# Optimization experiments

Measured on AMD Instinct MI355X. Metric: run time of the kernel, lower is better.

The kernel has to match this reference:

```python
import jax, jax.numpy as jnp
import numpy as np

N = 98304        # total nodes (= 16384 graphs * act_dim 6)
E = 1572864      # edges (avg degree 16)
C = 64           # in_channels
H = 32           # hidden_size
ACT = 6          # act_dim


def setup_inputs() -> dict:
    key = jax.random.key(0)
    ks = jax.random.split(key, 11)
    s = lambda fan: 1.0 / np.sqrt(fan)
    return {
        "state": jax.random.normal(ks[0], (N, C), jnp.float32),
        "edge_index": jax.random.randint(ks[1], (2, E), 0, N, dtype=jnp.int64),
        "conv_W": jax.random.normal(ks[2], (C, C), jnp.float32) * s(C),
        "conv_b": jax.random.normal(ks[3], (C,), jnp.float32) * 0.01,
        "W1": jax.random.normal(ks[4], (C, H), jnp.float32) * s(C),
        "b1": jax.random.normal(ks[5], (H,), jnp.float32) * 0.01,
        "W2": jax.random.normal(ks[6], (H, H), jnp.float32) * s(H),
        "b2": jax.random.normal(ks[7], (H,), jnp.float32) * 0.01,
        "W3": jax.random.normal(ks[8], (H, 1), jnp.float32) * s(H),
        "b3": jax.random.normal(ks[9], (1,), jnp.float32) * 0.01,
    }


def gcn_conv(x, edge_index, W, b):
    # PyG GCNConv: add self-loops, symmetric normalization D^-1/2 (A+I) D^-1/2 (X W) + b
    loops = jnp.arange(N, dtype=edge_index.dtype)
    src = jnp.concatenate([edge_index[0], loops])  # [E+N]
    dst = jnp.concatenate([edge_index[1], loops])  # [E+N]
    deg = jax.ops.segment_sum(jnp.ones(E + N, x.dtype), dst, num_segments=N)
    dinv = jax.lax.rsqrt(deg)                      # deg >= 1 due to self-loops
    norm = dinv[src] * dinv[dst]                   # [E+N]
    h = x @ W                                      # [N, C]
    msg = h[src] * norm[:, None]                   # gather + scale
    return jax.ops.segment_sum(msg, dst, num_segments=N) + b


def reference(state, edge_index, conv_W, conv_b, W1, b1, W2, b2, W3, b3):
    out = jax.nn.relu(gcn_conv(state, edge_index, conv_W, conv_b))
    x = out + state                                # residual
    x = x.reshape(-1, ACT, C)                      # [num_graphs, act_dim, C]
    x = jax.nn.relu(x @ W1 + b1)
    x = jax.nn.relu(x @ W2 + b2)
    x = jax.nn.softplus(x @ W3 + b3)
    concentration = x.squeeze(-1) + 1e-20          # [num_graphs, act_dim]
    return concentration
```

## Files before the change

### kernel.cpp

```cpp
#include <hip/hip_runtime.h>
#include <math.h>

#define Nn 98304
#define Ee 1572864
#define Cc 64
#define Hh 32
#define HB 256
#define EPB (Ee / HB)
#define NST 384
#define SN 256
#define CAP_ST 4800
#define GN 64


__device__ __forceinline__ int detect64(const void* ei) {
    const unsigned int* u = (const unsigned int*)ei;
    int is64 = 1;
    #pragma unroll
    for (int i = 0; i < 16; ++i) is64 &= (u[2 * i + 1] == 0u);
    return is64;
}

__device__ __forceinline__ int load_idx(const void* ei, long e, int is64) {
    if (is64) return (int)((const long long*)ei)[e];
    return ((const int*)ei)[e];
}

__device__ __forceinline__ unsigned short f2bf(float x) {
    union { float f; unsigned int u; } v; v.f = x;
    unsigned int r = v.u + 0x7FFFu + ((v.u >> 16) & 1u);
    return (unsigned short)(r >> 16);
}

__device__ __forceinline__ void acc_u4(float a[8], uint4 u) {
    union { unsigned int i; float f; } w;
    w.i = u.x << 16;         a[0] += w.f;
    w.i = u.x & 0xFFFF0000u; a[1] += w.f;
    w.i = u.y << 16;         a[2] += w.f;
    w.i = u.y & 0xFFFF0000u; a[3] += w.f;
    w.i = u.z << 16;         a[4] += w.f;
    w.i = u.z & 0xFFFF0000u; a[5] += w.f;
    w.i = u.w << 16;         a[6] += w.f;
    w.i = u.w & 0xFFFF0000u; a[7] += w.f;
}
__device__ __forceinline__ void set_u4(float a[8], uint4 u) {
    union { unsigned int i; float f; } w;
    w.i = u.x << 16;         a[0] = w.f;
    w.i = u.x & 0xFFFF0000u; a[1] = w.f;
    w.i = u.y << 16;         a[2] = w.f;
    w.i = u.y & 0xFFFF0000u; a[3] = w.f;
    w.i = u.z << 16;         a[4] = w.f;
    w.i = u.z & 0xFFFF0000u; a[5] = w.f;
    w.i = u.w << 16;         a[6] = w.f;
    w.i = u.w & 0xFFFF0000u; a[7] = w.f;
}

__global__ __launch_bounds__(1024) void k_p1(const void* __restrict__ ei,
                                             unsigned int* __restrict__ aux,
                                             unsigned int* __restrict__ ebuf) {
    __shared__ unsigned int hl[NST];
    __shared__ unsigned int cur[NST];
    int t = threadIdx.x, b = blockIdx.x;
    if (t < NST) hl[t] = 0;
    __syncthreads();
    int is64 = detect64(ei);
    long e0 = (long)b * EPB;
    #pragma unroll
    for (int i = 0; i < EPB / 1024; ++i) {
        int d = load_idx(ei, (long)Ee + e0 + i * 1024 + t, is64);
        atomicAdd(&hl[d >> 8], 1u);
    }
    __syncthreads();
    if (t < NST) cur[t] = hl[t];
    __syncthreads();
    for (int s = 1; s < NST; s <<= 1) {
        unsigned int v = (t < NST && t >= s) ? cur[t - s] : 0u;
        __syncthreads();
        if (t < NST) cur[t] += v;
        __syncthreads();
    }
    if (t < NST) {
        unsigned int ex = cur[t] - hl[t];
        aux[(long)b * NST + t] = ex | (hl[t] << 16);
        cur[t] = ex;
    }
    __syncthreads();
    #pragma unroll
    for (int i = 0; i < EPB / 1024; ++i) {
        long e = e0 + i * 1024 + t;
        int s = load_idx(ei, e, is64);
        int d = load_idx(ei, (long)Ee + e, is64);
        unsigned int pos = atomicAdd(&cur[d >> 8], 1u);
        ebuf[(long)b * EPB + pos] = (unsigned int)s | ((unsigned int)(d & (SN - 1)) << 17);
    }
}

__global__ __launch_bounds__(512) void k_p2(const unsigned int* __restrict__ aux,
                                            const unsigned int* __restrict__ ebuf,
                                            unsigned int* __restrict__ rowOff,
                                            unsigned int* __restrict__ rowEnd,
                                            float* __restrict__ dinv,
                                            unsigned int* __restrict__ srcs) {
    __shared__ unsigned int stage[CAP_ST];
    __shared__ unsigned int rbI[HB];
    __shared__ unsigned int rof[HB];
    __shared__ unsigned int cnt[SN];
    __shared__ unsigned int sc[SN];
    __shared__ unsigned int cur[SN];
    int t = threadIdx.x, st = blockIdx.x;
    if (t < HB) {
        unsigned int av = aux[(long)t * NST + st];
        rof[t] = av & 0xFFFFu;
        rbI[t] = av >> 16;
    }
    if (t < SN) cnt[t] = 0;
    __syncthreads();
    for (int s = 1; s < HB; s <<= 1) {
        unsigned int v = (t < HB && t >= s) ? rbI[t - s] : 0u;
        __syncthreads();
        if (t < HB) rbI[t] += v;
        __syncthreads();
    }
    int total = (int)rbI[HB - 1];
    for (int i = t; i < total; i += 512) {
        int lo = 0, hi = HB - 1;
        while (lo < hi) {
            int mid = (lo + hi) >> 1;
            if (rbI[mid] > (unsigned int)i) hi = mid; else lo = mid + 1;
        }
        unsigned int ex = lo ? rbI[lo - 1] : 0u;
        stage[i] = ebuf[(long)lo * EPB + rof[lo] + ((unsigned int)i - ex)];
    }
    __syncthreads();
    for (int i = t; i < total; i += 512)
        atomicAdd(&cnt[stage[i] >> 17], 1u);
    __syncthreads();
    if (t < SN) sc[t] = cnt[t];
    __syncthreads();
    #pragma unroll
    for (int off = 1; off < SN; off <<= 1) {
        unsigned int v = (t < SN && t >= off) ? sc[t - off] : 0u;
        __syncthreads();
        if (t < SN) sc[t] += v;
        __syncthreads();
    }
    if (t < SN) {
        unsigned int start = (unsigned int)(st * CAP_ST) + sc[t] - cnt[t];
        rowOff[(long)st * SN + t] = start;
        rowEnd[(long)st * SN + t] = start + cnt[t];
        cur[t] = start;
        dinv[(long)st * SN + t] = rsqrtf((float)(cnt[t] + 1));
    }
    __syncthreads();
    for (int i = t; i < total; i += 512) {
        unsigned int u = stage[i];
        unsigned int pos = atomicAdd(&cur[u >> 17], 1u);
        srcs[pos] = u & 0x1FFFFu;
    }
}

__global__ __launch_bounds__(256) void k_gemm(const float* __restrict__ state,
                                              const float* __restrict__ W,
                                              const float* __restrict__ dinv,
                                              unsigned short* __restrict__ gb) {
    __shared__ float Wl[64 * 64];
    __shared__ float Al[64 * 68];
    int t = threadIdx.x;
    long n0 = (long)blockIdx.x * 64;

    const float4* W4 = (const float4*)W;
    float4* Wl4 = (float4*)Wl;
    #pragma unroll
    for (int i = 0; i < 4; ++i) Wl4[i * 256 + t] = W4[i * 256 + t];

    const float4* S4 = (const float4*)(state) + n0 * 16;
    #pragma unroll
    for (int i = 0; i < 4; ++i) {
        int f4 = t + i * 256;
        int r = f4 >> 4, k0 = (f4 & 15) * 4;
        *(float4*)(Al + r * 68 + k0) = S4[f4];
    }
    __syncthreads();

    int r0 = (t >> 4) * 4;
    int c0 = (t & 15) * 4;
    float acc[4][4] = {{0.f}};
    #pragma unroll
    for (int kk = 0; kk < 64; kk += 4) {
        float4 a4[4], w4[4];
        #pragma unroll
        for (int i = 0; i < 4; ++i) a4[i] = *(const float4*)(Al + (r0 + i) * 68 + kk);
        #pragma unroll
        for (int j = 0; j < 4; ++j) w4[j] = *(const float4*)(Wl + (kk + j) * 64 + c0);
        const float* aa = (const float*)a4;
        const float* ww = (const float*)w4;
        #pragma unroll
        for (int i = 0; i < 4; ++i)
            #pragma unroll
            for (int j = 0; j < 4; ++j) {
                float av = aa[i * 4 + j];
                #pragma unroll
                for (int c = 0; c < 4; ++c)
                    acc[i][c] = fmaf(av, ww[j * 4 + c], acc[i][c]);
            }
    }
    #pragma unroll
    for (int i = 0; i < 4; ++i) {
        long n = n0 + r0 + i;
        float dv = dinv[n];
        ushort4 o;
        o.x = f2bf(acc[i][0] * dv); o.y = f2bf(acc[i][1] * dv);
        o.z = f2bf(acc[i][2] * dv); o.w = f2bf(acc[i][3] * dv);
        *(ushort4*)(gb + n * 64 + c0) = o;
    }
}

__global__ __launch_bounds__(512) void k_gf(const unsigned int* __restrict__ rowOff,
                                            const unsigned int* __restrict__ rowEnd,
                                            const unsigned int* __restrict__ srcs,
                                            const unsigned short* __restrict__ gb,
                                            const float* __restrict__ dinv,
                                            const float* __restrict__ state,
                                            const float* __restrict__ conv_b,
                                            const float* __restrict__ W1,
                                            const float* __restrict__ b1,
                                            const float* __restrict__ W2,
                                            const float* __restrict__ b2,
                                            const float* __restrict__ W3,
                                            const float* __restrict__ b3,
                                            float* __restrict__ out) {
    __shared__ float sa[GN * 68];
    __shared__ float hs[GN * 34];
    __shared__ float sW1[Cc * Hh];
    __shared__ float sW2[Hh * Hh];
    __shared__ float sW3[Hh], sb1[Hh], sb2[Hh], scb[Cc];
    __shared__ float sb3;
    int t = threadIdx.x;
    int wave = t >> 6, lane = t & 63;
    long n0 = (long)blockIdx.x * GN;

    for (int i = t; i < Cc * Hh; i += 512) sW1[i] = W1[i];
    for (int i = t; i < Hh * Hh; i += 512) sW2[i] = W2[i];
    if (t < Hh) { sW3[t] = W3[t]; sb1[t] = b1[t]; sb2[t] = b2[t]; }
    if (t >= 64 && t < 128) scb[t - 64] = conv_b[t - 64];
    if (t == 511) sb3 = b3[0];
    __syncthreads();

    {
        int g = lane >> 3;
        int cs = lane & 7;
        int j = wave * 8 + g;
        long n = n0 + j;
        int ptr = (int)rowOff[n];
        int end = (int)rowEnd[n];
        float dv = dinv[n];
        const uint4* gb4 = (const uint4*)gb;

        float a[8];
        set_u4(a, gb4[n * 8 + cs]);

        int cnt = end - ptr;
        uint4 r0, r1, r2, r3;
        if (cnt >= 4) {
            int s0 = (int)srcs[ptr];
            int s1 = (int)srcs[ptr + 1];
            int s2 = (int)srcs[ptr + 2];
            int s3 = (int)srcs[ptr + 3];
            r0 = gb4[(long)s0 * 8 + cs];
            r1 = gb4[(long)s1 * 8 + cs];
            r2 = gb4[(long)s2 * 8 + cs];
            r3 = gb4[(long)s3 * 8 + cs];
        }
        while (cnt >= 8) {
            int t0 = (int)srcs[ptr + 4];
            int t1 = (int)srcs[ptr + 5];
            int t2 = (int)srcs[ptr + 6];
            int t3 = (int)srcs[ptr + 7];
            acc_u4(a, r0); acc_u4(a, r1);
            acc_u4(a, r2); acc_u4(a, r3);
            r0 = gb4[(long)t0 * 8 + cs];
            r1 = gb4[(long)t1 * 8 + cs];
            r2 = gb4[(long)t2 * 8 + cs];
            r3 = gb4[(long)t3 * 8 + cs];
            ptr += 4; cnt -= 4;
        }
        if (cnt >= 4) {
            acc_u4(a, r0); acc_u4(a, r1);
            acc_u4(a, r2); acc_u4(a, r3);
            ptr += 4; cnt -= 4;
        }
        while (cnt > 0) {
            int s0 = (int)srcs[ptr];
            uint4 u0 = gb4[(long)s0 * 8 + cs];
            acc_u4(a, u0);
            ++ptr; --cnt;
        }

        float* r = sa + j * 68 + cs * 8;
        float4 lo, hi;
        lo.x = a[0] * dv; lo.y = a[1] * dv; lo.z = a[2] * dv; lo.w = a[3] * dv;
        hi.x = a[4] * dv; hi.y = a[5] * dv; hi.z = a[6] * dv; hi.w = a[7] * dv;
        *(float4*)r = lo;
        *(float4*)(r + 4) = hi;
    }
    __builtin_amdgcn_wave_barrier();

    {
        int j = t >> 3, o = t & 7;
        long n = n0 + j;
        int k0 = o * 8;
        const float4* sp4 = (const float4*)(state + n * 64 + k0);
        float4 s0 = sp4[0], s1 = sp4[1];
        float* r = sa + j * 68 + k0;
        r[0] = fmaxf(r[0] + scb[k0 + 0], 0.f) + s0.x;
        r[1] = fmaxf(r[1] + scb[k0 + 1], 0.f) + s0.y;
        r[2] = fmaxf(r[2] + scb[k0 + 2], 0.f) + s0.z;
        r[3] = fmaxf(r[3] + scb[k0 + 3], 0.f) + s0.w;
        r[4] = fmaxf(r[4] + scb[k0 + 4], 0.f) + s1.x;
        r[5] = fmaxf(r[5] + scb[k0 + 5], 0.f) + s1.y;
        r[6] = fmaxf(r[6] + scb[k0 + 6], 0.f) + s1.z;
        r[7] = fmaxf(r[7] + scb[k0 + 7], 0.f) + s1.w;
    }
    __builtin_amdgcn_wave_barrier();

    {
        int j = t >> 3, o = t & 7;
        int c0 = o * 4;
        float a0 = sb1[c0], a1 = sb1[c0 + 1], a2 = sb1[c0 + 2], a3 = sb1[c0 + 3];
        #pragma unroll
        for (int k = 0; k < Cc; ++k) {
            float xv = sa[j * 68 + k];
            float4 w = *(const float4*)(sW1 + k * Hh + c0);
            a0 = fmaf(xv, w.x, a0); a1 = fmaf(xv, w.y, a1);
            a2 = fmaf(xv, w.z, a2); a3 = fmaf(xv, w.w, a3);
        }
        float* r = hs + j * 34 + c0;
        r[0] = fmaxf(a0, 0.f); r[1] = fmaxf(a1, 0.f);
        r[2] = fmaxf(a2, 0.f); r[3] = fmaxf(a3, 0.f);
    }
    __builtin_amdgcn_wave_barrier();

    {
        int j = t >> 3, o = t & 7;
        int c0 = o * 4;
        float a0 = sb2[c0], a1 = sb2[c0 + 1], a2 = sb2[c0 + 2], a3 = sb2[c0 + 3];
        #pragma unroll
        for (int k = 0; k < Hh; ++k) {
            float xv = hs[j * 34 + k];
            float4 w = *(const float4*)(sW2 + k * Hh + c0);
            a0 = fmaf(xv, w.x, a0); a1 = fmaf(xv, w.y, a1);
            a2 = fmaf(xv, w.z, a2); a3 = fmaf(xv, w.w, a3);
        }
        float* r = sa + j * 68 + c0;
        r[0] = fmaxf(a0, 0.f); r[1] = fmaxf(a1, 0.f);
        r[2] = fmaxf(a2, 0.f); r[3] = fmaxf(a3, 0.f);
    }
    __builtin_amdgcn_wave_barrier();

    {
        int g = lane >> 3, o = lane & 7;
        int j = wave * 8 + g;
        int k0 = o * 4;
        float y = 0.f;
        #pragma unroll
        for (int k = 0; k < 4; ++k) y = fmaf(sa[j * 68 + k0 + k], sW3[k0 + k], y);
        y += __shfl_xor(y, 1, 64);
        y += __shfl_xor(y, 2, 64);
        y += __shfl_xor(y, 4, 64);
        if (o == 0) {
            y += sb3;
            float sp = fmaxf(y, 0.f) + log1pf(expf(-fabsf(y)));
            out[n0 + j] = sp + 1e-20f;
        }
    }
}

extern "C" void kernel_launch(void* const* d_in, const int* in_sizes, int n_in,
                              void* d_out, int out_size, void* d_ws, size_t ws_size,
                              hipStream_t stream) {
    const float* state  = (const float*)d_in[0];
    const void*  ei     = d_in[1];
    const float* conv_W = (const float*)d_in[2];
    const float* conv_b = (const float*)d_in[3];
    const float* W1 = (const float*)d_in[4];
    const float* b1 = (const float*)d_in[5];
    const float* W2 = (const float*)d_in[6];
    const float* b2 = (const float*)d_in[7];
    const float* W3 = (const float*)d_in[8];
    const float* b3 = (const float*)d_in[9];
    float* out = (float*)d_out;

    float*          dinv   = (float*)d_ws;
    unsigned short* gb     = (unsigned short*)(dinv + Nn);
    unsigned int*   rowOff = (unsigned int*)(gb + (size_t)Nn * 64);
    unsigned int*   rowEnd = rowOff + Nn;
    unsigned int*   aux    = rowEnd + Nn;
    unsigned int*   ebuf   = aux + (size_t)HB * NST;
    unsigned int*   srcs   = ebuf + Ee;

    k_p1<<<HB, 1024, 0, stream>>>(ei, aux, ebuf);
    k_p2<<<NST, 512, 0, stream>>>(aux, ebuf, rowOff, rowEnd, dinv, srcs);
    k_gemm<<<Nn / 64, 256, 0, stream>>>(state, conv_W, dinv, gb);
    k_gf<<<Nn / GN, 512, 0, stream>>>(rowOff, rowEnd, srcs, gb, dinv, state, conv_b,
                                      W1, b1, W2, b2, W3, b3, out);
}
```

Baseline: 172.1 us.

## Sort nodes by degree within block, deepen gather prefetch, use packed float2 accumulation

Each block now ranks its 64 nodes by in-degree and assigns them to wave lanes in sorted order, so the eight nodes sharing a wave have similar edge counts and less divergence. The gather loop now keeps two groups of four row loads in flight (eight outstanding) instead of one, to hide more memory latency. Accumulation uses 2-wide float vectors, which may let the compiler emit packed adds. The cost is an extra rank-sort phase, a block-wide barrier in place of the wave barrier, and higher register pressure.

```diff
diff --git a/kernel.cpp b/kernel.cpp
--- a/kernel.cpp
+++ b/kernel.cpp
@@ -12,6 +12,8 @@
 #define CAP_ST 4800
 #define GN 64
 
+typedef float v2f __attribute__((ext_vector_type(2)));
+
 
 __device__ __forceinline__ int detect64(const void* ei) {
     const unsigned int* u = (const unsigned int*)ei;
@@ -32,27 +34,17 @@
     return (unsigned short)(r >> 16);
 }
 
-__device__ __forceinline__ void acc_u4(float a[8], uint4 u) {
-    union { unsigned int i; float f; } w;
-    w.i = u.x << 16;         a[0] += w.f;
-    w.i = u.x & 0xFFFF0000u; a[1] += w.f;
-    w.i = u.y << 16;         a[2] += w.f;
-    w.i = u.y & 0xFFFF0000u; a[3] += w.f;
-    w.i = u.z << 16;         a[4] += w.f;
-    w.i = u.z & 0xFFFF0000u; a[5] += w.f;
-    w.i = u.w << 16;         a[6] += w.f;
-    w.i = u.w & 0xFFFF0000u; a[7] += w.f;
-}
-__device__ __forceinline__ void set_u4(float a[8], uint4 u) {
-    union { unsigned int i; float f; } w;
-    w.i = u.x << 16;         a[0] = w.f;
-    w.i = u.x & 0xFFFF0000u; a[1] = w.f;
-    w.i = u.y << 16;         a[2] = w.f;
-    w.i = u.y & 0xFFFF0000u; a[3] = w.f;
-    w.i = u.z << 16;         a[4] = w.f;
-    w.i = u.z & 0xFFFF0000u; a[5] = w.f;
-    w.i = u.w << 16;         a[6] = w.f;
-    w.i = u.w & 0xFFFF0000u; a[7] = w.f;
+__device__ __forceinline__ v2f up2(unsigned int u) {
+    union { unsigned int i; float f; } lo, hi;
+    lo.i = u << 16; hi.i = u & 0xFFFF0000u;
+    v2f r; r.x = lo.f; r.y = hi.f;
+    return r;
+}
+__device__ __forceinline__ void accv(v2f A[4], uint4 u) {
+    A[0] += up2(u.x); A[1] += up2(u.y); A[2] += up2(u.z); A[3] += up2(u.w);
+}
+__device__ __forceinline__ void setv(v2f A[4], uint4 u) {
+    A[0] = up2(u.x); A[1] = up2(u.y); A[2] = up2(u.z); A[3] = up2(u.w);
 }
 
 __global__ __launch_bounds__(1024) void k_p1(const void* __restrict__ ei,
@@ -235,6 +227,8 @@
     __shared__ float sW2[Hh * Hh];
     __shared__ float sW3[Hh], sb1[Hh], sb2[Hh], scb[Cc];
     __shared__ float sb3;
+    __shared__ int deg[GN];
+    __shared__ unsigned short perm[GN];
     int t = threadIdx.x;
     int wave = t >> 6, lane = t & 63;
     long n0 = (long)blockIdx.x * GN;
@@ -244,66 +238,94 @@
     if (t < Hh) { sW3[t] = W3[t]; sb1[t] = b1[t]; sb2[t] = b2[t]; }
     if (t >= 64 && t < 128) scb[t - 64] = conv_b[t - 64];
     if (t == 511) sb3 = b3[0];
+    if (t < GN) deg[t] = (int)(rowEnd[n0 + t] - rowOff[n0 + t]);
+    __syncthreads();
+
+    if (t < GN) {
+        int d = deg[t], r = 0;
+        #pragma unroll
+        for (int k = 0; k < GN; ++k) {
+            int dk = deg[k];
+            r += (dk > d || (dk == d && k < t)) ? 1 : 0;
+        }
+        perm[r] = (unsigned short)t;
+    }
     __syncthreads();
 
     {
-        int g = lane >> 3;
+        int G = wave * 8 + (lane >> 3);
         int cs = lane & 7;
-        int j = wave * 8 + g;
-        long n = n0 + j;
+        int jn = (int)perm[G];
+        long n = n0 + jn;
         int ptr = (int)rowOff[n];
         int end = (int)rowEnd[n];
         float dv = dinv[n];
         const uint4* gb4 = (const uint4*)gb;
 
-        float a[8];
-        set_u4(a, gb4[n * 8 + cs]);
+        v2f A[4];
+        setv(A, gb4[n * 8 + cs]);
 
         int cnt = end - ptr;
-        uint4 r0, r1, r2, r3;
+        uint4 r0, r1, r2, r3, q0, q1, q2, q3;
         if (cnt >= 4) {
-            int s0 = (int)srcs[ptr];
-            int s1 = (int)srcs[ptr + 1];
-            int s2 = (int)srcs[ptr + 2];
-            int s3 = (int)srcs[ptr + 3];
-            r0 = gb4[(long)s0 * 8 + cs];
-            r1 = gb4[(long)s1 * 8 + cs];
-            r2 = gb4[(long)s2 * 8 + cs];
-            r3 = gb4[(long)s3 * 8 + cs];
-        }
-        while (cnt >= 8) {
-            int t0 = (int)srcs[ptr + 4];
-            int t1 = (int)srcs[ptr + 5];
-            int t2 = (int)srcs[ptr + 6];
-            int t3 = (int)srcs[ptr + 7];
-            acc_u4(a, r0); acc_u4(a, r1);
-            acc_u4(a, r2); acc_u4(a, r3);
-            r0 = gb4[(long)t0 * 8 + cs];
-            r1 = gb4[(long)t1 * 8 + cs];
-            r2 = gb4[(long)t2 * 8 + cs];
-            r3 = gb4[(long)t3 * 8 + cs];
-            ptr += 4; cnt -= 4;
-        }
-        if (cnt >= 4) {
-            acc_u4(a, r0); acc_u4(a, r1);
-            acc_u4(a, r2); acc_u4(a, r3);
+            int s0 = (int)srcs[ptr],     s1 = (int)srcs[ptr + 1];
+            int s2 = (int)srcs[ptr + 2], s3 = (int)srcs[ptr + 3];
+            r0 = gb4[(long)s0 * 8 + cs]; r1 = gb4[(long)s1 * 8 + cs];
+            r2 = gb4[(long)s2 * 8 + cs]; r3 = gb4[(long)s3 * 8 + cs];
+        }
+        if (cnt >= 8) {
+            int s0 = (int)srcs[ptr + 4], s1 = (int)srcs[ptr + 5];
+            int s2 = (int)srcs[ptr + 6], s3 = (int)srcs[ptr + 7];
+            q0 = gb4[(long)s0 * 8 + cs]; q1 = gb4[(long)s1 * 8 + cs];
+            q2 = gb4[(long)s2 * 8 + cs]; q3 = gb4[(long)s3 * 8 + cs];
+        }
+        while (cnt >= 16) {
+            int a0 = (int)srcs[ptr + 8],  a1 = (int)srcs[ptr + 9];
+            int a2 = (int)srcs[ptr + 10], a3 = (int)srcs[ptr + 11];
+            accv(A, r0); accv(A, r1); accv(A, r2); accv(A, r3);
+            r0 = gb4[(long)a0 * 8 + cs]; r1 = gb4[(long)a1 * 8 + cs];
+            r2 = gb4[(long)a2 * 8 + cs]; r3 = gb4[(long)a3 * 8 + cs];
+            int b0 = (int)srcs[ptr + 12], b1_ = (int)srcs[ptr + 13];
+            int b2_ = (int)srcs[ptr + 14], b3_ = (int)srcs[ptr + 15];
+            accv(A, q0); accv(A, q1); accv(A, q2); accv(A, q3);
+            q0 = gb4[(long)b0 * 8 + cs];  q1 = gb4[(long)b1_ * 8 + cs];
+            q2 = gb4[(long)b2_ * 8 + cs]; q3 = gb4[(long)b3_ * 8 + cs];
+            ptr += 8; cnt -= 8;
+        }
+        if (cnt >= 12) {
+            int a0 = (int)srcs[ptr + 8],  a1 = (int)srcs[ptr + 9];
+            int a2 = (int)srcs[ptr + 10], a3 = (int)srcs[ptr + 11];
+            accv(A, r0); accv(A, r1); accv(A, r2); accv(A, r3);
+            r0 = gb4[(long)a0 * 8 + cs]; r1 = gb4[(long)a1 * 8 + cs];
+            r2 = gb4[(long)a2 * 8 + cs]; r3 = gb4[(long)a3 * 8 + cs];
+            accv(A, q0); accv(A, q1); accv(A, q2); accv(A, q3);
+            accv(A, r0); accv(A, r1); accv(A, r2); accv(A, r3);
+            ptr += 12; cnt -= 12;
+        } else if (cnt >= 8) {
+            accv(A, r0); accv(A, r1); accv(A, r2); accv(A, r3);
+            accv(A, q0); accv(A, q1); accv(A, q2); accv(A, q3);
+            ptr += 8; cnt -= 8;
+        } else if (cnt >= 4) {
+            accv(A, r0); accv(A, r1); accv(A, r2); accv(A, r3);
             ptr += 4; cnt -= 4;
         }
         while (cnt > 0) {
             int s0 = (int)srcs[ptr];
             uint4 u0 = gb4[(long)s0 * 8 + cs];
-            acc_u4(a, u0);
+            accv(A, u0);
             ++ptr; --cnt;
         }
 
-        float* r = sa + j * 68 + cs * 8;
+        float* r = sa + jn * 68 + cs * 8;
         float4 lo, hi;
-        lo.x = a[0] * dv; lo.y = a[1] * dv; lo.z = a[2] * dv; lo.w = a[3] * dv;
-        hi.x = a[4] * dv; hi.y = a[5] * dv; hi.z = a[6] * dv; hi.w = a[7] * dv;
+        lo.x = A[0].x * dv; lo.y = A[0].y * dv;
+        lo.z = A[1].x * dv; lo.w = A[1].y * dv;
+        hi.x = A[2].x * dv; hi.y = A[2].y * dv;
+        hi.z = A[3].x * dv; hi.w = A[3].y * dv;
         *(float4*)r = lo;
         *(float4*)(r + 4) = hi;
     }
-    __builtin_amdgcn_wave_barrier();
+    __syncthreads();
 
     {
         int j = t >> 3, o = t & 7;
```

Result: slower. 182.1 us (+5.8%).
